# Optimization experiments

Hardware: AMD Instinct MI355X
Metric: run time of the kernel (lower is better)

## Reference

```python
import jax, jax.numpy as jnp
import numpy as np

N_HEADS = 8
DIM_HEAD = 64
SCALE = DIM_HEAD ** -0.5


def setup_inputs() -> dict:
    key = jax.random.key(0)
    ks = jax.random.split(key, 7)
    B, C, H, W = 2, 512, 64, 64
    inner = N_HEADS * DIM_HEAD  # 512
    x = jax.random.normal(ks[0], (B, C, H, W), dtype=jnp.float32)
    context = jax.random.normal(ks[1], (B, C, H, W), dtype=jnp.float32)
    # kaiming_normal fan_out for 1x1 conv: std = sqrt(2 / out_channels)
    std_qkv = (2.0 / inner) ** 0.5
    std_o = (2.0 / C) ** 0.5
    Wq = jax.random.normal(ks[2], (inner, C), dtype=jnp.float32) * std_qkv
    Wk = jax.random.normal(ks[3], (inner, C), dtype=jnp.float32) * std_qkv
    Wv = jax.random.normal(ks[4], (inner, C), dtype=jnp.float32) * std_qkv
    Wo = jax.random.normal(ks[5], (C, inner), dtype=jnp.float32) * std_o
    return {
        'x': x, 'context': context,
        'Wq': Wq, 'bq': jnp.zeros((inner,), jnp.float32),
        'Wk': Wk, 'bk': jnp.zeros((inner,), jnp.float32),
        'Wv': Wv, 'bv': jnp.zeros((inner,), jnp.float32),
        'Wo': Wo, 'bo': jnp.zeros((C,), jnp.float32),
    }


def _attention(x, context, Wq, bq, Wk, bk, Wv, bv, Wo, bo):
    b, c, h, w = x.shape
    s = h * w
    # 1x1 conv == per-pixel channel matmul. Flatten spatial: [b, s, c]
    xf = x.reshape(b, c, s).transpose(0, 2, 1)
    cf = context.reshape(b, c, s).transpose(0, 2, 1)
    q = jnp.einsum('bsc,ec->bse', xf, Wq) + bq  # [b, s, inner]
    k = jnp.einsum('bsc,ec->bse', cf, Wk) + bk
    v = jnp.einsum('bsc,ec->bse', cf, Wv) + bv
    # split heads: [b, n, s, d]
    def split(t):
        return t.reshape(b, s, N_HEADS, DIM_HEAD).transpose(0, 2, 1, 3)
    q, k, v = split(q), split(k), split(v)
    sim = jnp.einsum('bnid,bnjd->bnij', q, k) * SCALE  # [b, n, s, s]
    attn = jax.nn.softmax(sim, axis=-1)
    out = jnp.einsum('bnij,bnjd->bnid', attn, v)  # [b, n, s, d]
    # merge heads back to channels: 'b n s d -> b (n d) s'
    out = out.transpose(0, 2, 1, 3).reshape(b, s, N_HEADS * DIM_HEAD)
    out = jnp.einsum('bse,ce->bsc', out, Wo) + bo  # output proj (1x1 conv)
    return out.transpose(0, 2, 1).reshape(b, c, h, w)


def reference(x, context, Wq, bq, Wk, bk, Wv, bv, Wo, bo):
    return _attention(x, context, Wq, bq, Wk, bk, Wv, bv, Wo, bo)
```

## Files before the change

### kernel.cpp

```cpp
#include <hip/hip_runtime.h>
#include <cstdint>


typedef __bf16 bf16x8 __attribute__((ext_vector_type(8)));
typedef __bf16 bf16x4 __attribute__((ext_vector_type(4)));
typedef float f32x4 __attribute__((ext_vector_type(4)));
typedef unsigned short u16x8 __attribute__((ext_vector_type(8)));
typedef unsigned short u16x4 __attribute__((ext_vector_type(4)));

#define AS1 __attribute__((address_space(1)))
#define AS3 __attribute__((address_space(3)))

__device__ __forceinline__ void async16(const void* g, void* l) {
  __builtin_amdgcn_global_load_lds((const AS1 void*)g, (AS3 void*)l, 16, 0, 0);
}

__device__ __forceinline__ uint16_t f2bf(float f) {
  union { float f; uint32_t u; } a;
  a.f = f;
  uint32_t r = a.u + 0x7fffu + ((a.u >> 16) & 1u);
  return (uint16_t)(r >> 16);
}

__device__ __forceinline__ float bf2f(uint16_t u) {
  union { uint32_t u; float f; } a;
  a.u = (uint32_t)u << 16;
  return a.f;
}

__global__ __launch_bounds__(256) void cvt_w(
    const float* __restrict__ W0, const float* __restrict__ W1,
    const float* __restrict__ W2, const float* __restrict__ W3,
    uint16_t* __restrict__ O0, uint16_t* __restrict__ O1,
    uint16_t* __restrict__ O2, uint16_t* __restrict__ O3) {
  const float* W[4] = {W0, W1, W2, W3};
  uint16_t* O[4] = {O0, O1, O2, O3};
  const int w = blockIdx.y;
  const int i = (blockIdx.x * 256 + threadIdx.x) * 4;
  float4 v = *(const float4*)&W[w][i];
  u16x4 o = {f2bf(v.x), f2bf(v.y), f2bf(v.z), f2bf(v.w)};
  *(u16x4*)&O[w][i] = o;
}

__global__ __launch_bounds__(256) void transpose_cs(
    const float* __restrict__ x, const float* __restrict__ ctx,
    uint16_t* __restrict__ xT, uint16_t* __restrict__ cT) {
  const int zz = blockIdx.z;
  const float* src = (zz < 2 ? x : ctx) + (size_t)(zz & 1) * 512 * 4096;
  uint16_t* dst = (zz < 2 ? xT : cT) + (size_t)(zz & 1) * 4096 * 512;
  const int s0 = blockIdx.x * 64, c0 = blockIdx.y * 64;
  __shared__ uint16_t tile[64][80];
  const int t = threadIdx.x;
  for (int p = 0; p < 2; ++p) {
    int u = p * 256 + t;
    int r = u >> 3, cg = (u & 7) * 8;
    const float* sp = &src[(size_t)(c0 + r) * 4096 + s0 + cg];
    float4 v0 = *(const float4*)sp;
    float4 v1 = *(const float4*)(sp + 4);
    u16x8 o = {f2bf(v0.x), f2bf(v0.y), f2bf(v0.z), f2bf(v0.w),
               f2bf(v1.x), f2bf(v1.y), f2bf(v1.z), f2bf(v1.w)};
    *(u16x8*)&tile[r][cg] = o;
  }
  __syncthreads();
  for (int p = 0; p < 2; ++p) {
    int u = p * 256 + t;
    int sr = u >> 3, cg = (u & 7) * 8;
    u16x8 v;
    for (int j = 0; j < 8; ++j) v[j] = tile[cg + j][sr];
    *(u16x8*)&dst[(size_t)(s0 + sr) * 512 + c0 + cg] = v;
  }
}

struct QkvArgs {
  const uint16_t* A[3]; long long sA[3];
  const uint16_t* B[3]; long long sB[3];
  uint16_t* C[3];       long long sC[3];
  const float* bias[3];
  float os[3];
  int N[3]; int lx[3]; int brow[3];
};

__global__ __launch_bounds__(256) void gemm_qkv(QkvArgs ga) {
  constexpr int K = 512;
  __shared__ uint16_t At[128 * 32];
  __shared__ uint16_t Bt[128 * 32];
  const int t = threadIdx.x, lane = t & 63, wave = t >> 6;
  const int lr = lane & 15, lq = lane >> 4;
  const int wm = (wave >> 1) * 64, wn = (wave & 1) * 64;
  const int sel = blockIdx.z >> 1, bat = blockIdx.z & 1;
  const int lx = ga.lx[sel], N = ga.N[sel], brow = ga.brow[sel];
  const float os = ga.os[sel];
  const int n0 = (blockIdx.x & ((1 << lx) - 1)) * 128;
  const int m0 = (blockIdx.x >> lx) * 128;
  const uint16_t* A = ga.A[sel] + (size_t)bat * ga.sA[sel];
  const uint16_t* B = ga.B[sel] + (size_t)bat * ga.sB[sel];
  const float* bias = ga.bias[sel];
  f32x4 acc[4][4] = {};
  for (int k0 = 0; k0 < K; k0 += 32) {
    __syncthreads();
    for (int p = 0; p < 2; ++p) {
      int u = p * 256 + t;
      int r = u >> 2, c = (u & 3) * 8;
      async16(&A[(size_t)(m0 + r) * K + k0 + c], &At[p * 2048 + wave * 512]);
      async16(&B[(size_t)(n0 + r) * K + k0 + c], &Bt[p * 2048 + wave * 512]);
    }
    __syncthreads();
    bf16x8 af[4], bfr[4];
    for (int i = 0; i < 4; ++i)
      af[i] = *(const bf16x8*)&At[(wm + i * 16 + lr) * 32 + lq * 8];
    for (int j = 0; j < 4; ++j)
      bfr[j] = *(const bf16x8*)&Bt[(wn + j * 16 + lr) * 32 + lq * 8];
    for (int i = 0; i < 4; ++i)
      for (int j = 0; j < 4; ++j)
        acc[i][j] = __builtin_amdgcn_mfma_f32_16x16x32_bf16(af[i], bfr[j], acc[i][j], 0, 0, 0);
  }
  uint16_t* C = ga.C[sel] + (size_t)bat * ga.sC[sel];
  for (int i = 0; i < 4; ++i)
    for (int j = 0; j < 4; ++j) {
      int row = m0 + wm + i * 16 + lq * 4;
      int col = n0 + wn + j * 16 + lr;
      float bc = brow ? 0.f : bias[col];
      for (int r = 0; r < 4; ++r) {
        float val = (acc[i][j][r] + (brow ? bias[row + r] : bc)) * os;
        C[(size_t)(row + r) * N + col] = f2bf(val);
      }
    }
}

__global__ __launch_bounds__(256) void gemm_out(
    const uint16_t* __restrict__ Wo, const uint16_t* __restrict__ Ob,
    long long sB, float* __restrict__ Y, long long sC, int N,
    const float* __restrict__ bias) {
  constexpr int K = 512;
  __shared__ uint16_t At[64 * 32];
  __shared__ uint16_t Bt[128 * 32];
  const int t = threadIdx.x, lane = t & 63, wave = t >> 6;
  const int lr = lane & 15, lq = lane >> 4;
  const int wm = (wave >> 1) * 32, wn = (wave & 1) * 64;
  const int m0 = blockIdx.y * 64, n0 = blockIdx.x * 128;
  const uint16_t* B = Ob + (size_t)blockIdx.z * sB;
  f32x4 acc[2][4] = {};
  for (int k0 = 0; k0 < K; k0 += 32) {
    __syncthreads();
    {
      int r = t >> 2, c = (t & 3) * 8;
      async16(&Wo[(size_t)(m0 + r) * K + k0 + c], &At[wave * 512]);
    }
    for (int p = 0; p < 2; ++p) {
      int u = p * 256 + t;
      int r = u >> 2, c = (u & 3) * 8;
      async16(&B[(size_t)(n0 + r) * K + k0 + c], &Bt[p * 2048 + wave * 512]);
    }
    __syncthreads();
    bf16x8 af[2], bfr[4];
    for (int i = 0; i < 2; ++i)
      af[i] = *(const bf16x8*)&At[(wm + i * 16 + lr) * 32 + lq * 8];
    for (int j = 0; j < 4; ++j)
      bfr[j] = *(const bf16x8*)&Bt[(wn + j * 16 + lr) * 32 + lq * 8];
    for (int i = 0; i < 2; ++i)
      for (int j = 0; j < 4; ++j)
        acc[i][j] = __builtin_amdgcn_mfma_f32_16x16x32_bf16(af[i], bfr[j], acc[i][j], 0, 0, 0);
  }
  float* Cf = Y + (size_t)blockIdx.z * sC;
  for (int i = 0; i < 2; ++i)
    for (int j = 0; j < 4; ++j) {
      int row = m0 + wm + i * 16 + lq * 4;
      int col = n0 + wn + j * 16 + lr;
      for (int r = 0; r < 4; ++r)
        Cf[(size_t)(row + r) * N + col] = acc[i][j][r] + bias[row + r];
    }
}

__global__ __launch_bounds__(512, 4) void attn128(
    const uint16_t* __restrict__ Q, const uint16_t* __restrict__ K,
    const uint16_t* __restrict__ Vt, uint16_t* __restrict__ Ap,
    float* __restrict__ Lp) {
  constexpr int S = 4096, E = 512;
  const int b = blockIdx.z & 1, jh = blockIdx.z >> 1;
  const int h = blockIdx.y;
  const int i0 = blockIdx.x * 256;
  const int t = threadIdx.x, lane = t & 63, wave = t >> 6;
  const int lr = lane & 15, lq = lane >> 4;
  const size_t qkB = (size_t)b * S * E;
  const size_t vB = (size_t)b * E * S;
  __shared__ uint16_t Kl[64 * 64];
  __shared__ uint16_t Vl[64 * 64];
  __shared__ __bf16 Pl[8 * 2 * 16 * 72];

  const int qbase = i0 + wave * 32;
  bf16x8 qf[2][2];
  for (int g = 0; g < 2; ++g) {
    const size_t qo = qkB + (size_t)(qbase + g * 16 + lr) * E + h * 64 + lq * 8;
    qf[g][0] = *(const bf16x8*)&Q[qo];
    qf[g][1] = *(const bf16x8*)&Q[qo + 32];
  }
  f32x4 lsum[2] = {};
  f32x4 accOT[2][4] = {};
  const int swz = (lr & 7);
  const int srr = t >> 3, ssc = ((t & 7) ^ (srr & 7)) * 8;

  const int jbeg = jh * (S / 2), jend = jbeg + S / 2;
  for (int j0 = jbeg; j0 < jend; j0 += 64) {
    __syncthreads();
    async16(&K[qkB + (size_t)(j0 + srr) * E + h * 64 + ssc], &Kl[wave * 512]);
    async16(&Vt[vB + (size_t)(h * 64 + srr) * S + j0 + ssc], &Vl[wave * 512]);
    __builtin_amdgcn_s_waitcnt(0);
    __syncthreads();
    f32x4 svt[2][4];
    for (int jn = 0; jn < 4; ++jn) {
      const int row = jn * 16 + lr;
      const int c0 = (lq ^ swz) * 8;
      bf16x8 ka0 = *(const bf16x8*)&Kl[row * 64 + c0];
      bf16x8 ka1 = *(const bf16x8*)&Kl[row * 64 + (c0 ^ 32)];
      for (int g = 0; g < 2; ++g) {
        f32x4 z = {0.f, 0.f, 0.f, 0.f};
        z = __builtin_amdgcn_mfma_f32_16x16x32_bf16(ka0, qf[g][0], z, 0, 0, 0);
        z = __builtin_amdgcn_mfma_f32_16x16x32_bf16(ka1, qf[g][1], z, 0, 0, 0);
        svt[g][jn] = z;
      }
    }
    for (int g = 0; g < 2; ++g) {
      __bf16* pr = &Pl[((wave * 2 + g) * 16 + lr) * 72];
      for (int jn = 0; jn < 4; ++jn) {
        f32x4 p;
        for (int r = 0; r < 4; ++r) p[r] = exp2f(svt[g][jn][r]);
        lsum[g] += p;
        bf16x4 pk;
        for (int r = 0; r < 4; ++r) pk[r] = (__bf16)p[r];
        *(bf16x4*)&pr[jn * 16 + lq * 4] = pk;
      }
    }
    bf16x8 pa[2][2];
    for (int g = 0; g < 2; ++g) {
      const __bf16* pr = &Pl[((wave * 2 + g) * 16 + lr) * 72];
      pa[g][0] = *(const bf16x8*)&pr[lq * 8];
      pa[g][1] = *(const bf16x8*)&pr[32 + lq * 8];
    }
    for (int dn = 0; dn < 4; ++dn) {
      const int row = dn * 16 + lr;
      const int c0 = (lq ^ swz) * 8;
      bf16x8 v0 = *(const bf16x8*)&Vl[row * 64 + c0];
      bf16x8 v1 = *(const bf16x8*)&Vl[row * 64 + (c0 ^ 32)];
      for (int g = 0; g < 2; ++g) {
        accOT[g][dn] = __builtin_amdgcn_mfma_f32_16x16x32_bf16(v0, pa[g][0], accOT[g][dn], 0, 0, 0);
        accOT[g][dn] = __builtin_amdgcn_mfma_f32_16x16x32_bf16(v1, pa[g][1], accOT[g][dn], 0, 0, 0);
      }
    }
  }
  uint16_t* Aph = Ap + (size_t)jh * 2 * S * E;
  float* Lph = Lp + ((size_t)(jh * 2 + b) * 8 + h) * S;
  for (int g = 0; g < 2; ++g) {
    float lt = (lsum[g][0] + lsum[g][1]) + (lsum[g][2] + lsum[g][3]);
    lt += __shfl_xor(lt, 16);
    lt += __shfl_xor(lt, 32);
    if (lane < 16) Lph[qbase + g * 16 + lr] = lt;
    const size_t row = qbase + g * 16 + lr;
    for (int dn = 0; dn < 4; ++dn) {
      u16x4 o;
      for (int r = 0; r < 4; ++r) o[r] = f2bf(accOT[g][dn][r]);
      *(u16x4*)&Aph[qkB + row * E + h * 64 + dn * 16 + lq * 4] = o;
    }
  }
}

__global__ __launch_bounds__(256) void attn_combine(
    const uint16_t* __restrict__ Ap, const float* __restrict__ Lp,
    uint16_t* __restrict__ Ob) {
  constexpr int S = 4096, E = 512;
  const size_t HALF = (size_t)2 * S * E;
  const size_t idx = ((size_t)blockIdx.x * 256 + threadIdx.x) * 4;
  const int b = (int)(idx / ((size_t)S * E));
  const size_t rem = idx % ((size_t)S * E);
  const int s = (int)(rem / E), e = (int)(rem % E);
  const int h = e >> 6;
  const float l0 = Lp[((size_t)(0 * 2 + b) * 8 + h) * S + s];
  const float l1 = Lp[((size_t)(1 * 2 + b) * 8 + h) * S + s];
  const float inv = 1.f / (l0 + l1);
  u16x4 a0 = *(const u16x4*)&Ap[idx];
  u16x4 a1 = *(const u16x4*)&Ap[HALF + idx];
  u16x4 o;
  for (int r = 0; r < 4; ++r) o[r] = f2bf((bf2f(a0[r]) + bf2f(a1[r])) * inv);
  *(u16x4*)&Ob[idx] = o;
}

extern "C" void kernel_launch(void* const* d_in, const int* in_sizes, int n_in,
                              void* d_out, int out_size, void* d_ws, size_t ws_size,
                              hipStream_t stream) {
  const float* x   = (const float*)d_in[0];
  const float* ctx = (const float*)d_in[1];
  const float* Wq  = (const float*)d_in[2];
  const float* bq  = (const float*)d_in[3];
  const float* Wk  = (const float*)d_in[4];
  const float* bk  = (const float*)d_in[5];
  const float* Wv  = (const float*)d_in[6];
  const float* bv  = (const float*)d_in[7];
  const float* Wo  = (const float*)d_in[8];
  const float* bo  = (const float*)d_in[9];
  float* out = (float*)d_out;

  const size_t SZ = (size_t)2 * 4096 * 512;
  uint16_t* xT = (uint16_t*)d_ws;
  uint16_t* cT = xT + SZ;
  uint16_t* Qb = cT + SZ;
  uint16_t* Kb = Qb + SZ;
  uint16_t* Vb = Kb + SZ;
  uint16_t* Ob = Vb + SZ;
  uint16_t* Wqb = Ob + SZ;
  uint16_t* Wkb = Wqb + 512 * 512;
  uint16_t* Wvb = Wkb + 512 * 512;
  uint16_t* Wob = Wvb + 512 * 512;
  uint16_t* Ap  = Wob + 512 * 512;
  float*    Lp  = (float*)(Ap + 2 * SZ);
  const long long sIn = 4096LL * 512LL;
  const float slh = 0.125f * 1.44269504088896f;

  cvt_w<<<dim3(256, 4), 256, 0, stream>>>(Wq, Wk, Wv, Wo, Wqb, Wkb, Wvb, Wob);
  transpose_cs<<<dim3(64, 8, 4), 256, 0, stream>>>(x, ctx, xT, cT);
  QkvArgs qkv = {
      {xT, cT, Wvb}, {sIn, sIn, 0},
      {Wqb, Wkb, cT}, {0, 0, sIn},
      {Qb, Kb, Vb}, {sIn, sIn, sIn},
      {bq, bk, bv},
      {slh, 1.f, 1.f},
      {512, 512, 4096}, {2, 2, 5}, {0, 0, 1}};
  gemm_qkv<<<dim3(128, 1, 6), 256, 0, stream>>>(qkv);
  attn128<<<dim3(16, 8, 4), 512, 0, stream>>>(Qb, Kb, Vb, Ap, Lp);
  attn_combine<<<dim3(4096), 256, 0, stream>>>(Ap, Lp, Ob);
  gemm_out<<<dim3(32, 8, 2), 256, 0, stream>>>(Wob, Ob, sIn, out, sIn, 4096, bo);
}
```

Baseline: 251.1 us.

## Double-buffer K/V tiles in attention and vectorize transposed GEMM epilogue stores

The attention kernel now double-buffers the K and V tiles in LDS. It prefetches the next 64-key tile while computing on the current one, which hides global-load latency behind the MFMA work. The QKV and output GEMMs swap their A/B operand roles so each lane writes four contiguous outputs as one vector store (u16x4 / float4) instead of scattered scalar stores. Explicit waitcnts are added before barriers. The cost is double the K/V LDS footprint, which may lower occupancy for the 512-thread attention blocks.

```diff
diff --git a/kernel.cpp b/kernel.cpp
--- a/kernel.cpp
+++ b/kernel.cpp
@@ -77,7 +77,7 @@
   uint16_t* C[3];       long long sC[3];
   const float* bias[3];
   float os[3];
-  int N[3]; int lx[3]; int brow[3];
+  long long ldC[3]; int lx[3]; int brow[3];
 };
 
 __global__ __launch_bounds__(256) void gemm_qkv(QkvArgs ga) {
@@ -88,7 +88,8 @@
   const int lr = lane & 15, lq = lane >> 4;
   const int wm = (wave >> 1) * 64, wn = (wave & 1) * 64;
   const int sel = blockIdx.z >> 1, bat = blockIdx.z & 1;
-  const int lx = ga.lx[sel], N = ga.N[sel], brow = ga.brow[sel];
+  const int lx = ga.lx[sel], brow = ga.brow[sel];
+  const long long ldC = ga.ldC[sel];
   const float os = ga.os[sel];
   const int n0 = (blockIdx.x & ((1 << lx) - 1)) * 128;
   const int m0 = (blockIdx.x >> lx) * 128;
@@ -104,6 +105,7 @@
       async16(&A[(size_t)(m0 + r) * K + k0 + c], &At[p * 2048 + wave * 512]);
       async16(&B[(size_t)(n0 + r) * K + k0 + c], &Bt[p * 2048 + wave * 512]);
     }
+    __builtin_amdgcn_s_waitcnt(0);
     __syncthreads();
     bf16x8 af[4], bfr[4];
     for (int i = 0; i < 4; ++i)
@@ -120,54 +122,59 @@
       int row = m0 + wm + i * 16 + lq * 4;
       int col = n0 + wn + j * 16 + lr;
       float bc = brow ? 0.f : bias[col];
+      u16x4 o;
       for (int r = 0; r < 4; ++r) {
         float val = (acc[i][j][r] + (brow ? bias[row + r] : bc)) * os;
-        C[(size_t)(row + r) * N + col] = f2bf(val);
+        o[r] = f2bf(val);
       }
+      *(u16x4*)&C[(size_t)col * ldC + row] = o;
     }
 }
 
 __global__ __launch_bounds__(256) void gemm_out(
-    const uint16_t* __restrict__ Wo, const uint16_t* __restrict__ Ob,
-    long long sB, float* __restrict__ Y, long long sC, int N,
+    const uint16_t* __restrict__ Ob, long long sA,
+    const uint16_t* __restrict__ Wo, float* __restrict__ Y, long long sC,
     const float* __restrict__ bias) {
   constexpr int K = 512;
-  __shared__ uint16_t At[64 * 32];
-  __shared__ uint16_t Bt[128 * 32];
+  __shared__ uint16_t At[128 * 32];
+  __shared__ uint16_t Bt[64 * 32];
   const int t = threadIdx.x, lane = t & 63, wave = t >> 6;
   const int lr = lane & 15, lq = lane >> 4;
-  const int wm = (wave >> 1) * 32, wn = (wave & 1) * 64;
-  const int m0 = blockIdx.y * 64, n0 = blockIdx.x * 128;
-  const uint16_t* B = Ob + (size_t)blockIdx.z * sB;
-  f32x4 acc[2][4] = {};
+  const int wm = (wave & 1) * 64, wn = (wave >> 1) * 32;
+  const int m0 = blockIdx.y * 128, n0 = blockIdx.x * 64;
+  const uint16_t* A = Ob + (size_t)blockIdx.z * sA;
+  f32x4 acc[4][2] = {};
   for (int k0 = 0; k0 < K; k0 += 32) {
     __syncthreads();
-    {
-      int r = t >> 2, c = (t & 3) * 8;
-      async16(&Wo[(size_t)(m0 + r) * K + k0 + c], &At[wave * 512]);
-    }
     for (int p = 0; p < 2; ++p) {
       int u = p * 256 + t;
       int r = u >> 2, c = (u & 3) * 8;
-      async16(&B[(size_t)(n0 + r) * K + k0 + c], &Bt[p * 2048 + wave * 512]);
-    }
-    __syncthreads();
-    bf16x8 af[2], bfr[4];
-    for (int i = 0; i < 2; ++i)
+      async16(&A[(size_t)(m0 + r) * K + k0 + c], &At[p * 2048 + wave * 512]);
+    }
+    {
+      int r = t >> 2, c = (t & 3) * 8;
+      async16(&Wo[(size_t)(n0 + r) * K + k0 + c], &Bt[wave * 512]);
+    }
+    __builtin_amdgcn_s_waitcnt(0);
+    __syncthreads();
+    bf16x8 af[4], bfr[2];
+    for (int i = 0; i < 4; ++i)
       af[i] = *(const bf16x8*)&At[(wm + i * 16 + lr) * 32 + lq * 8];
-    for (int j = 0; j < 4; ++j)
+    for (int j = 0; j < 2; ++j)
       bfr[j] = *(const bf16x8*)&Bt[(wn + j * 16 + lr) * 32 + lq * 8];
-    for (int i = 0; i < 2; ++i)
-      for (int j = 0; j < 4; ++j)
+    for (int i = 0; i < 4; ++i)
+      for (int j = 0; j < 2; ++j)
         acc[i][j] = __builtin_amdgcn_mfma_f32_16x16x32_bf16(af[i], bfr[j], acc[i][j], 0, 0, 0);
   }
   float* Cf = Y + (size_t)blockIdx.z * sC;
-  for (int i = 0; i < 2; ++i)
-    for (int j = 0; j < 4; ++j) {
+  for (int i = 0; i < 4; ++i)
+    for (int j = 0; j < 2; ++j) {
       int row = m0 + wm + i * 16 + lq * 4;
       int col = n0 + wn + j * 16 + lr;
-      for (int r = 0; r < 4; ++r)
-        Cf[(size_t)(row + r) * N + col] = acc[i][j][r] + bias[row + r];
+      float bb = bias[col];
+      float4 o = {acc[i][j][0] + bb, acc[i][j][1] + bb,
+                  acc[i][j][2] + bb, acc[i][j][3] + bb};
+      *(float4*)&Cf[(size_t)col * 4096 + row] = o;
     }
 }
 
@@ -183,8 +190,8 @@
   const int lr = lane & 15, lq = lane >> 4;
   const size_t qkB = (size_t)b * S * E;
   const size_t vB = (size_t)b * E * S;
-  __shared__ uint16_t Kl[64 * 64];
-  __shared__ uint16_t Vl[64 * 64];
+  __shared__ uint16_t Kl[2][64 * 64];
+  __shared__ uint16_t Vl[2][64 * 64];
   __shared__ __bf16 Pl[8 * 2 * 16 * 72];
 
   const int qbase = i0 + wave * 32;
@@ -200,18 +207,25 @@
   const int srr = t >> 3, ssc = ((t & 7) ^ (srr & 7)) * 8;
 
   const int jbeg = jh * (S / 2), jend = jbeg + S / 2;
+  async16(&K[qkB + (size_t)(jbeg + srr) * E + h * 64 + ssc], &Kl[0][wave * 512]);
+  async16(&Vt[vB + (size_t)(h * 64 + srr) * S + jbeg + ssc], &Vl[0][wave * 512]);
+  __builtin_amdgcn_s_waitcnt(0);
+  __syncthreads();
+
+  int cur = 0;
   for (int j0 = jbeg; j0 < jend; j0 += 64) {
-    __syncthreads();
-    async16(&K[qkB + (size_t)(j0 + srr) * E + h * 64 + ssc], &Kl[wave * 512]);
-    async16(&Vt[vB + (size_t)(h * 64 + srr) * S + j0 + ssc], &Vl[wave * 512]);
-    __builtin_amdgcn_s_waitcnt(0);
-    __syncthreads();
+    if (j0 + 64 < jend) {
+      async16(&K[qkB + (size_t)(j0 + 64 + srr) * E + h * 64 + ssc], &Kl[cur ^ 1][wave * 512]);
+      async16(&Vt[vB + (size_t)(h * 64 + srr) * S + j0 + 64 + ssc], &Vl[cur ^ 1][wave * 512]);
+    }
+    const uint16_t* Kc = Kl[cur];
+    const uint16_t* Vc = Vl[cur];
     f32x4 svt[2][4];
     for (int jn = 0; jn < 4; ++jn) {
       const int row = jn * 16 + lr;
       const int c0 = (lq ^ swz) * 8;
-      bf16x8 ka0 = *(const bf16x8*)&Kl[row * 64 + c0];
-      bf16x8 ka1 = *(const bf16x8*)&Kl[row * 64 + (c0 ^ 32)];
+      bf16x8 ka0 = *(const bf16x8*)&Kc[row * 64 + c0];
+      bf16x8 ka1 = *(const bf16x8*)&Kc[row * 64 + (c0 ^ 32)];
       for (int g = 0; g < 2; ++g) {
         f32x4 z = {0.f, 0.f, 0.f, 0.f};
         z = __builtin_amdgcn_mfma_f32_16x16x32_bf16(ka0, qf[g][0], z, 0, 0, 0);
@@ -239,13 +253,16 @@
     for (int dn = 0; dn < 4; ++dn) {
       const int row = dn * 16 + lr;
       const int c0 = (lq ^ swz) * 8;
-      bf16x8 v0 = *(const bf16x8*)&Vl[row * 64 + c0];
-      bf16x8 v1 = *(const bf16x8*)&Vl[row * 64 + (c0 ^ 32)];
+      bf16x8 v0 = *(const bf16x8*)&Vc[row * 64 + c0];
+      bf16x8 v1 = *(const bf16x8*)&Vc[row * 64 + (c0 ^ 32)];
       for (int g = 0; g < 2; ++g) {
         accOT[g][dn] = __builtin_amdgcn_mfma_f32_16x16x32_bf16(v0, pa[g][0], accOT[g][dn], 0, 0, 0);
         accOT[g][dn] = __builtin_amdgcn_mfma_f32_16x16x32_bf16(v1, pa[g][1], accOT[g][dn], 0, 0, 0);
       }
     }
+    __builtin_amdgcn_s_waitcnt(0);
+    __syncthreads();
+    cur ^= 1;
   }
   uint16_t* Aph = Ap + (size_t)jh * 2 * S * E;
   float* Lph = Lp + ((size_t)(jh * 2 + b) * 8 + h) * S;
@@ -317,14 +334,16 @@
   cvt_w<<<dim3(256, 4), 256, 0, stream>>>(Wq, Wk, Wv, Wo, Wqb, Wkb, Wvb, Wob);
   transpose_cs<<<dim3(64, 8, 4), 256, 0, stream>>>(x, ctx, xT, cT);
   QkvArgs qkv = {
+      {Wqb, Wkb, cT}, {0, 0, sIn},
       {xT, cT, Wvb}, {sIn, sIn, 0},
-      {Wqb, Wkb, cT}, {0, 0, sIn},
       {Qb, Kb, Vb}, {sIn, sIn, sIn},
       {bq, bk, bv},
       {slh, 1.f, 1.f},
-      {512, 512, 4096}, {2, 2, 5}, {0, 0, 1}};
+      {512, 512, 4096},
+      {5, 5, 2},
+      {1, 1, 0}};
   gemm_qkv<<<dim3(128, 1, 6), 256, 0, stream>>>(qkv);
   attn128<<<dim3(16, 8, 4), 512, 0, stream>>>(Qb, Kb, Vb, Ap, Lp);
   attn_combine<<<dim3(4096), 256, 0, stream>>>(Ap, Lp, Ob);
-  gemm_out<<<dim3(32, 8, 2), 256, 0, stream>>>(Wob, Ob, sIn, out, sIn, 4096, bo);
-}
+  gemm_out<<<dim3(8, 32, 2), 256, 0, stream>>>(Ob, sIn, Wob, out, sIn, bo);
+}
```

Measured after the change: 247.6 us, median of 2. About the same (-1.4%).
